# Kernel tuning notes

Hardware: AMD Instinct MI355X
Metric: run time of the kernel (lower is better)

The kernel has to match this reference:

```python
import jax, jax.numpy as jnp
import numpy as np

B, T, IN, H = 512, 1024, 1, 64


def setup_inputs() -> dict:
    key = jax.random.key(0)
    ks = jax.random.split(key, 7)
    s = 1.0 / np.sqrt(H)  # PyTorch LSTM init range
    u = lambda k, shape: jax.random.uniform(k, shape, jnp.float32, -s, s)
    return {
        "x": jax.random.normal(ks[0], (B, T, IN), jnp.float32),
        "W_ih": u(ks[1], (4 * H, IN)),
        "W_hh": u(ks[2], (4 * H, H)),
        "b_ih": u(ks[3], (4 * H,)),
        "b_hh": u(ks[4], (4 * H,)),
        "W_lin": u(ks[5], (1, H)),
        "b_lin": u(ks[6], (1,)),
    }


def reference(x, W_ih, W_hh, b_ih, b_hh, W_lin, b_lin):
    # x: [B, T, IN] (batch_first). Identity quantizers => plain LSTM math.
    Bsz = x.shape[0]
    Hs = W_hh.shape[1]
    bias = b_ih + b_hh  # fold the two bias vectors once
    xs = jnp.swapaxes(x, 0, 1)  # [T, B, IN] for scan over time
    h0 = jnp.zeros((Bsz, Hs), x.dtype)
    c0 = jnp.zeros((Bsz, Hs), x.dtype)

    def step(carry, xt):
        h, c = carry
        gates = xt @ W_ih.T + h @ W_hh.T + bias  # [B, 4H]
        i, f, g, o = jnp.split(gates, 4, axis=-1)  # PyTorch gate order i,f,g,o
        i = jax.nn.sigmoid(i)
        f = jax.nn.sigmoid(f)
        g = jnp.tanh(g)
        o = jax.nn.sigmoid(o)
        c_new = f * c + i * g
        h_new = o * jnp.tanh(c_new)
        return (h_new, c_new), None

    (h_final, _), _ = jax.lax.scan(step, (h0, c0), xs)
    # final_hidden_states.squeeze(0) -> [B, H]; linear -> [B, 1]; view(-1) -> [B]
    return (h_final @ W_lin.T + b_lin).reshape(-1)
```

## Files before the change

### kernel.cpp

```cpp
#include <hip/hip_runtime.h>


#define TLEN 1024
#define HID  64

__device__ __forceinline__ float fast_sigmoid(float x) {
    return __builtin_amdgcn_rcpf(1.0f + __expf(-x));
}
__device__ __forceinline__ float fast_tanh(float x) {
    return __builtin_fmaf(2.0f, fast_sigmoid(2.0f * x), -1.0f);
}

__global__ __launch_bounds__(256, 2)
void qlstm_kernel(const float* __restrict__ x,
                  const float* __restrict__ W_ih,
                  const float* __restrict__ W_hh,
                  const float* __restrict__ b_ih,
                  const float* __restrict__ b_hh,
                  const float* __restrict__ W_lin,
                  const float* __restrict__ b_lin,
                  float* __restrict__ out)
{
    const int b   = blockIdx.x;
    const int tid = threadIdx.x;
    const int w   = tid >> 6;
    const int l   = tid & 63;

    __shared__ __align__(16) float xs[TLEN];
    __shared__ __align__(16) float hs4[4][HID];
    __shared__ __align__(16) float act[2][4][HID];

    ((float4*)xs)[tid] = ((const float4*)(x + (size_t)b * TLEN))[tid];

    const int row = w * HID + l;
    const float4* Wr = (const float4*)(W_hh + (size_t)row * HID);
    float4 wq[16];
    #pragma unroll
    for (int q = 0; q < 16; ++q) wq[q] = Wr[q];

    const float u    = W_ih[row];
    const float bias = b_ih[row] + b_hh[row];
    const float wlin = W_lin[l];

    float c = 0.0f, h = 0.0f;
    hs4[w][l] = 0.0f;
    __syncthreads();

    for (int t = 0; t < TLEN; ++t) {
        const int p = t & 1;
        const float xt = xs[t];

        float acc = __builtin_fmaf(xt, u, bias);
        #pragma unroll
        for (int q = 0; q < 16; ++q) {
            const float4 hk = *(const float4*)&hs4[w][4 * q];
            acc = __builtin_fmaf(hk.x, wq[q].x, acc);
            acc = __builtin_fmaf(hk.y, wq[q].y, acc);
            acc = __builtin_fmaf(hk.z, wq[q].z, acc);
            acc = __builtin_fmaf(hk.w, wq[q].w, acc);
        }

        const float a = (w == 2) ? fast_tanh(acc) : fast_sigmoid(acc);
        act[p][w][l] = a;
        __syncthreads();

        const float ai = act[p][0][l];
        const float af = act[p][1][l];
        const float ag = act[p][2][l];
        const float ao = act[p][3][l];
        c = __builtin_fmaf(af, c, ai * ag);
        h = ao * fast_tanh(c);
        hs4[w][l] = h;
    }

    if (w == 0) {
        float v = h * wlin;
        #pragma unroll
        for (int off = 32; off > 0; off >>= 1)
            v += __shfl_down(v, off, 64);
        if (l == 0) out[b] = v + b_lin[0];
    }
}

extern "C" void kernel_launch(void* const* d_in, const int* in_sizes, int n_in,
                              void* d_out, int out_size, void* d_ws, size_t ws_size,
                              hipStream_t stream) {
    const float* x     = (const float*)d_in[0];
    const float* W_ih  = (const float*)d_in[1];
    const float* W_hh  = (const float*)d_in[2];
    const float* b_ih  = (const float*)d_in[3];
    const float* b_hh  = (const float*)d_in[4];
    const float* W_lin = (const float*)d_in[5];
    const float* b_lin = (const float*)d_in[6];
    float* out = (float*)d_out;

    const int B = out_size;
    qlstm_kernel<<<B, 256, 0, stream>>>(x, W_ih, W_hh, b_ih, b_hh, W_lin, b_lin, out);
}
```

Measured before the change: 584.3 us.

## Split each gate dot product across two half-waves with 512 threads per block

Doubles the block to 512 threads so each gate row's 64-long dot product over h is split between two half-wavefronts of 32 lanes, combined with a cross-lane xor shuffle. Each lane keeps half as many W_hh registers and uses four independent accumulators to shorten the serial FMA chain per step. Activations are stored as interleaved [HID][4] so the cell update reads all four gates with one float4 load. The cost is extra shuffle and wave overhead plus redundant cell-state computation across eight waves, and lower occupancy headroom from 512-thread blocks.

```diff
diff --git a/kernel.cpp b/kernel.cpp
--- a/kernel.cpp
+++ b/kernel.cpp
@@ -11,7 +11,7 @@
     return __builtin_fmaf(2.0f, fast_sigmoid(2.0f * x), -1.0f);
 }
 
-__global__ __launch_bounds__(256, 2)
+__global__ __launch_bounds__(512, 4)
 void qlstm_kernel(const float* __restrict__ x,
                   const float* __restrict__ W_ih,
                   const float* __restrict__ W_hh,
@@ -25,52 +25,73 @@
     const int tid = threadIdx.x;
     const int w   = tid >> 6;
     const int l   = tid & 63;
+    const int lr  = l & 31;
+    const int kh  = l >> 5;
+    const int g   = w >> 1;
+    const int row = w * 32 + lr;
+    const int k0  = kh * 32;
 
     __shared__ __align__(16) float xs[TLEN];
-    __shared__ __align__(16) float hs4[4][HID];
-    __shared__ __align__(16) float act[2][4][HID];
+    __shared__ __align__(16) float hs[8][HID];
+    __shared__ __align__(16) float act[2][HID][4];
 
-    ((float4*)xs)[tid] = ((const float4*)(x + (size_t)b * TLEN))[tid];
+    ((float2*)xs)[tid] = ((const float2*)(x + (size_t)b * TLEN))[tid];
 
-    const int row = w * HID + l;
-    const float4* Wr = (const float4*)(W_hh + (size_t)row * HID);
-    float4 wq[16];
+    const float4* Wr = (const float4*)(W_hh + (size_t)row * HID + k0);
+    float4 wq[8];
     #pragma unroll
-    for (int q = 0; q < 16; ++q) wq[q] = Wr[q];
+    for (int q = 0; q < 8; ++q) wq[q] = Wr[q];
 
     const float u    = W_ih[row];
     const float bias = b_ih[row] + b_hh[row];
     const float wlin = W_lin[l];
 
     float c = 0.0f, h = 0.0f;
-    hs4[w][l] = 0.0f;
+    hs[w][l] = 0.0f;
     __syncthreads();
 
     for (int t = 0; t < TLEN; ++t) {
         const int p = t & 1;
         const float xt = xs[t];
+        const float base = __builtin_fmaf(xt, u, bias);
 
-        float acc = __builtin_fmaf(xt, u, bias);
+        float acc0 = (kh == 0) ? base : 0.0f;
+        float acc1 = 0.0f, acc2 = 0.0f, acc3 = 0.0f;
         #pragma unroll
-        for (int q = 0; q < 16; ++q) {
-            const float4 hk = *(const float4*)&hs4[w][4 * q];
-            acc = __builtin_fmaf(hk.x, wq[q].x, acc);
-            acc = __builtin_fmaf(hk.y, wq[q].y, acc);
-            acc = __builtin_fmaf(hk.z, wq[q].z, acc);
-            acc = __builtin_fmaf(hk.w, wq[q].w, acc);
+        for (int q = 0; q < 8; q += 4) {
+            const float4 ha = *(const float4*)&hs[w][k0 + 4 * (q + 0)];
+            const float4 hb = *(const float4*)&hs[w][k0 + 4 * (q + 1)];
+            const float4 hc = *(const float4*)&hs[w][k0 + 4 * (q + 2)];
+            const float4 hd = *(const float4*)&hs[w][k0 + 4 * (q + 3)];
+            acc0 = __builtin_fmaf(ha.x, wq[q + 0].x, acc0);
+            acc0 = __builtin_fmaf(ha.y, wq[q + 0].y, acc0);
+            acc0 = __builtin_fmaf(ha.z, wq[q + 0].z, acc0);
+            acc0 = __builtin_fmaf(ha.w, wq[q + 0].w, acc0);
+            acc1 = __builtin_fmaf(hb.x, wq[q + 1].x, acc1);
+            acc1 = __builtin_fmaf(hb.y, wq[q + 1].y, acc1);
+            acc1 = __builtin_fmaf(hb.z, wq[q + 1].z, acc1);
+            acc1 = __builtin_fmaf(hb.w, wq[q + 1].w, acc1);
+            acc2 = __builtin_fmaf(hc.x, wq[q + 2].x, acc2);
+            acc2 = __builtin_fmaf(hc.y, wq[q + 2].y, acc2);
+            acc2 = __builtin_fmaf(hc.z, wq[q + 2].z, acc2);
+            acc2 = __builtin_fmaf(hc.w, wq[q + 2].w, acc2);
+            acc3 = __builtin_fmaf(hd.x, wq[q + 3].x, acc3);
+            acc3 = __builtin_fmaf(hd.y, wq[q + 3].y, acc3);
+            acc3 = __builtin_fmaf(hd.z, wq[q + 3].z, acc3);
+            acc3 = __builtin_fmaf(hd.w, wq[q + 3].w, acc3);
         }
+        float accv = (acc0 + acc1) + (acc2 + acc3);
+        accv += __shfl_xor(accv, 32, 64);
 
-        const float a = (w == 2) ? fast_tanh(acc) : fast_sigmoid(acc);
-        act[p][w][l] = a;
+        const float a = (g == 2) ? fast_tanh(accv) : fast_sigmoid(accv);
+        if (lr == l)
+            act[p][(w & 1) * 32 + lr][g] = a;
         __syncthreads();
 
-        const float ai = act[p][0][l];
-        const float af = act[p][1][l];
-        const float ag = act[p][2][l];
-        const float ao = act[p][3][l];
-        c = __builtin_fmaf(af, c, ai * ag);
-        h = ao * fast_tanh(c);
-        hs4[w][l] = h;
+        const float4 a4 = *(const float4*)&act[p][l][0];
+        c = __builtin_fmaf(a4.y, c, a4.x * a4.z);
+        h = a4.w * fast_tanh(c);
+        hs[w][l] = h;
     }
 
     if (w == 0) {
@@ -95,5 +116,5 @@
     float* out = (float*)d_out;
 
     const int B = out_size;
-    qlstm_kernel<<<B, 256, 0, stream>>>(x, W_ih, W_hh, b_ih, b_hh, W_lin, b_lin, out);
+    qlstm_kernel<<<B, 512, 0, stream>>>(x, W_ih, W_hh, b_ih, b_hh, W_lin, b_lin, out);
 }
```

Measured after the change: 605.7 us. 3.7% more time.

## Remap gate rows so each wave owns whole units and exchange gates via shuffles

Applied to the files above, without the earlier changes.

Each wave now holds all four gates for 16 hidden units, so the i/f/g/o values are gathered within the wave with cross-lane shuffles. This replaces the shared-memory act buffer and lets the loop drop one of its two barriers per step. The hidden state is double-buffered in a single shared array, and the dot product uses packed 2-wide FMAs with four independent accumulators to shorten the dependency chain. The gate activation is made branchless through per-lane scale and offset constants. The cost is that all four lane groups compute the cell update redundantly and extra shuffle instructions sit on the serial critical path.

```diff
diff --git a/kernel.cpp b/kernel.cpp
--- a/kernel.cpp
+++ b/kernel.cpp
@@ -1,14 +1,13 @@
 #include <hip/hip_runtime.h>
 
+
+typedef float v2f __attribute__((ext_vector_type(2)));
 
 #define TLEN 1024
 #define HID  64
 
 __device__ __forceinline__ float fast_sigmoid(float x) {
     return __builtin_amdgcn_rcpf(1.0f + __expf(-x));
-}
-__device__ __forceinline__ float fast_tanh(float x) {
-    return __builtin_fmaf(2.0f, fast_sigmoid(2.0f * x), -1.0f);
 }
 
 __global__ __launch_bounds__(256, 2)
@@ -21,60 +20,82 @@
                   const float* __restrict__ b_lin,
                   float* __restrict__ out)
 {
-    const int b   = blockIdx.x;
-    const int tid = threadIdx.x;
-    const int w   = tid >> 6;
-    const int l   = tid & 63;
+    const int b    = blockIdx.x;
+    const int tid  = threadIdx.x;
+    const int w    = tid >> 6;
+    const int l    = tid & 63;
+    const int u16  = l & 15;
+    const int gt   = l >> 4;
+    const int unit = w * 16 + u16;
+    const int row  = gt * HID + unit;
 
     __shared__ __align__(16) float xs[TLEN];
-    __shared__ __align__(16) float hs4[4][HID];
-    __shared__ __align__(16) float act[2][4][HID];
+    __shared__ __align__(16) float hs[2][HID];
 
     ((float4*)xs)[tid] = ((const float4*)(x + (size_t)b * TLEN))[tid];
 
-    const int row = w * HID + l;
-    const float4* Wr = (const float4*)(W_hh + (size_t)row * HID);
-    float4 wq[16];
+    v2f w2[32];
+    const v2f* Wr = (const v2f*)(W_hh + (size_t)row * HID);
     #pragma unroll
-    for (int q = 0; q < 16; ++q) wq[q] = Wr[q];
+    for (int q = 0; q < 32; ++q) w2[q] = Wr[q];
 
-    const float u    = W_ih[row];
+    const float uw   = W_ih[row];
     const float bias = b_ih[row] + b_hh[row];
-    const float wlin = W_lin[l];
 
-    float c = 0.0f, h = 0.0f;
-    hs4[w][l] = 0.0f;
+    const bool  isg = (gt == 2);
+    const float s_  = isg ? 2.0f : 1.0f;
+    const float m_  = isg ? 2.0f : 1.0f;
+    const float d_  = isg ? -1.0f : 0.0f;
+    const bool  lead = (gt == 0);
+    const bool  fi   = (gt < 2);
+
+    float c = 0.0f;
+    if (tid < HID) hs[0][tid] = 0.0f;
     __syncthreads();
 
     for (int t = 0; t < TLEN; ++t) {
         const int p = t & 1;
         const float xt = xs[t];
+        const float base = __builtin_fmaf(xt, uw, bias);
 
-        float acc = __builtin_fmaf(xt, u, bias);
+        v2f a0 = {base, 0.0f}, a1 = {0.0f, 0.0f}, a2 = {0.0f, 0.0f}, a3 = {0.0f, 0.0f};
+        const float4* hp = (const float4*)&hs[p][0];
         #pragma unroll
-        for (int q = 0; q < 16; ++q) {
-            const float4 hk = *(const float4*)&hs4[w][4 * q];
-            acc = __builtin_fmaf(hk.x, wq[q].x, acc);
-            acc = __builtin_fmaf(hk.y, wq[q].y, acc);
-            acc = __builtin_fmaf(hk.z, wq[q].z, acc);
-            acc = __builtin_fmaf(hk.w, wq[q].w, acc);
+        for (int q = 0; q < 16; q += 2) {
+            const float4 h0 = hp[q];
+            const float4 h1 = hp[q + 1];
+            const v2f hA = {h0.x, h0.y}, hB = {h0.z, h0.w};
+            const v2f hC = {h1.x, h1.y}, hD = {h1.z, h1.w};
+            a0 = __builtin_elementwise_fma(hA, w2[2 * q + 0], a0);
+            a1 = __builtin_elementwise_fma(hB, w2[2 * q + 1], a1);
+            a2 = __builtin_elementwise_fma(hC, w2[2 * q + 2], a2);
+            a3 = __builtin_elementwise_fma(hD, w2[2 * q + 3], a3);
         }
+        const v2f s2 = (a0 + a1) + (a2 + a3);
+        const float acc = s2.x + s2.y;
 
-        const float a = (w == 2) ? fast_tanh(acc) : fast_sigmoid(acc);
-        act[p][w][l] = a;
+        const float a = __builtin_fmaf(m_, fast_sigmoid(s_ * acc), d_);
+
+        const float b16  = __shfl_xor(a, 16, 64);
+        const float lo   = (gt & 1) ? b16 : a;
+        const float hi   = (gt & 1) ? a   : b16;
+        const float lo32 = __shfl_xor(lo, 32, 64);
+        const float hi32 = __shfl_xor(hi, 32, 64);
+        const float ig = fi ? lo   : lo32;
+        const float fg = fi ? hi   : hi32;
+        const float gg = fi ? lo32 : lo;
+        const float og = fi ? hi32 : hi;
+
+        c = __builtin_fmaf(fg, c, ig * gg);
+        const float th = __builtin_fmaf(2.0f, fast_sigmoid(2.0f * c), -1.0f);
+        const float h  = og * th;
+        if (lead) hs[p ^ 1][unit] = h;
+
         __syncthreads();
-
-        const float ai = act[p][0][l];
-        const float af = act[p][1][l];
-        const float ag = act[p][2][l];
-        const float ao = act[p][3][l];
-        c = __builtin_fmaf(af, c, ai * ag);
-        h = ao * fast_tanh(c);
-        hs4[w][l] = h;
     }
 
     if (w == 0) {
-        float v = h * wlin;
+        float v = hs[0][l] * W_lin[l];
         #pragma unroll
         for (int off = 32; off > 0; off >>= 1)
             v += __shfl_down(v, off, 64);
```

After: 606.2 us. +3.7%, slower.

## Use two-wave blocks with readlane h broadcast and packed FMA gate matvec

Applied to the files above, without the earlier changes.

Shrinks each block from four wavefronts (one per gate) to two, with each lane computing two gate rows held in registers as packed pairs. The hidden state is broadcast with readlane into scalar registers instead of going through LDS, and the matvec uses v_pk_fma_f32 with scalar operands, split across four accumulators. Only activations are exchanged between the two waves via LDS, which cuts shared-memory traffic and halves the waves taking part in each barrier. The cost is 64 readlanes per step, double the per-lane register footprint, and lower occupancy.

```diff
diff --git a/kernel.cpp b/kernel.cpp
--- a/kernel.cpp
+++ b/kernel.cpp
@@ -1,5 +1,7 @@
 #include <hip/hip_runtime.h>
 
+
+typedef float v2f __attribute__((ext_vector_type(2)));
 
 #define TLEN 1024
 #define HID  64
@@ -11,7 +13,7 @@
     return __builtin_fmaf(2.0f, fast_sigmoid(2.0f * x), -1.0f);
 }
 
-__global__ __launch_bounds__(256, 2)
+__global__ __launch_bounds__(128, 1)
 void qlstm_kernel(const float* __restrict__ x,
                   const float* __restrict__ W_ih,
                   const float* __restrict__ W_hh,
@@ -26,51 +28,84 @@
     const int w   = tid >> 6;
     const int l   = tid & 63;
 
-    __shared__ __align__(16) float xs[TLEN];
-    __shared__ __align__(16) float hs4[4][HID];
-    __shared__ __align__(16) float act[2][4][HID];
+    __shared__ __align__(16) float  xs[TLEN];
+    __shared__ __align__(8)  float2 axc[2][2][HID];
 
-    ((float4*)xs)[tid] = ((const float4*)(x + (size_t)b * TLEN))[tid];
+    {
+        const float4* xsrc = (const float4*)(x + (size_t)b * TLEN);
+        ((float4*)xs)[tid]       = xsrc[tid];
+        ((float4*)xs)[128 + tid] = xsrc[128 + tid];
+    }
 
-    const int row = w * HID + l;
-    const float4* Wr = (const float4*)(W_hh + (size_t)row * HID);
-    float4 wq[16];
-    #pragma unroll
-    for (int q = 0; q < 16; ++q) wq[q] = Wr[q];
+    const int r0 = (2 * w) * HID + l;
+    const int r1 = (2 * w + 1) * HID + l;
+    v2f wg2[64];
+    {
+        const float4* p0 = (const float4*)(W_hh + (size_t)r0 * HID);
+        const float4* p1 = (const float4*)(W_hh + (size_t)r1 * HID);
+        #pragma unroll
+        for (int k4 = 0; k4 < 16; ++k4) {
+            const float4 a = p0[k4];
+            const float4 c4 = p1[k4];
+            wg2[4 * k4 + 0] = (v2f){a.x, c4.x};
+            wg2[4 * k4 + 1] = (v2f){a.y, c4.y};
+            wg2[4 * k4 + 2] = (v2f){a.z, c4.z};
+            wg2[4 * k4 + 3] = (v2f){a.w, c4.w};
+        }
+    }
 
-    const float u    = W_ih[row];
-    const float bias = b_ih[row] + b_hh[row];
+    const v2f u2    = (v2f){W_ih[r0], W_ih[r1]};
+    const v2f bias2 = (v2f){b_ih[r0] + b_hh[r0], b_ih[r1] + b_hh[r1]};
     const float wlin = W_lin[l];
 
+    const float sA = (w == 1) ? 2.0f : 1.0f;
+    const float mA = (w == 1) ? 2.0f : 1.0f;
+    const float dA = (w == 1) ? -1.0f : 0.0f;
+
     float c = 0.0f, h = 0.0f;
-    hs4[w][l] = 0.0f;
     __syncthreads();
 
     for (int t = 0; t < TLEN; ++t) {
         const int p = t & 1;
         const float xt = xs[t];
 
-        float acc = __builtin_fmaf(xt, u, bias);
+        const int hbits = __float_as_int(h);
+        v2f hp[32];
         #pragma unroll
-        for (int q = 0; q < 16; ++q) {
-            const float4 hk = *(const float4*)&hs4[w][4 * q];
-            acc = __builtin_fmaf(hk.x, wq[q].x, acc);
-            acc = __builtin_fmaf(hk.y, wq[q].y, acc);
-            acc = __builtin_fmaf(hk.z, wq[q].z, acc);
-            acc = __builtin_fmaf(hk.w, wq[q].w, acc);
+        for (int q = 0; q < 32; ++q) {
+            hp[q].x = __int_as_float(__builtin_amdgcn_readlane(hbits, 2 * q));
+            hp[q].y = __int_as_float(__builtin_amdgcn_readlane(hbits, 2 * q + 1));
         }
 
-        const float a = (w == 2) ? fast_tanh(acc) : fast_sigmoid(acc);
-        act[p][w][l] = a;
+        v2f a0 = {0.0f, 0.0f}, a1 = {0.0f, 0.0f};
+        v2f a2 = {0.0f, 0.0f}, a3 = {0.0f, 0.0f};
+        #pragma unroll
+        for (int q = 0; q < 32; q += 2) {
+            asm("v_pk_fma_f32 %0, %1, %2, %0 op_sel:[0,0,0] op_sel_hi:[0,1,1]"
+                : "+v"(a0) : "s"(hp[q]),     "v"(wg2[2 * q + 0]));
+            asm("v_pk_fma_f32 %0, %1, %2, %0 op_sel:[1,0,0] op_sel_hi:[1,1,1]"
+                : "+v"(a1) : "s"(hp[q]),     "v"(wg2[2 * q + 1]));
+            asm("v_pk_fma_f32 %0, %1, %2, %0 op_sel:[0,0,0] op_sel_hi:[0,1,1]"
+                : "+v"(a2) : "s"(hp[q + 1]), "v"(wg2[2 * q + 2]));
+            asm("v_pk_fma_f32 %0, %1, %2, %0 op_sel:[1,0,0] op_sel_hi:[1,1,1]"
+                : "+v"(a3) : "s"(hp[q + 1]), "v"(wg2[2 * q + 3]));
+        }
+        v2f gate = (a0 + a1) + (a2 + a3);
+        gate.x = __builtin_fmaf(xt, u2.x, gate.x + bias2.x);
+        gate.y = __builtin_fmaf(xt, u2.y, gate.y + bias2.y);
+
+        const float ax = __builtin_fmaf(mA, fast_sigmoid(sA * gate.x), dA);
+        const float ay = fast_sigmoid(gate.y);
+
+        axc[p][w][l] = make_float2(ax, ay);
         __syncthreads();
-
-        const float ai = act[p][0][l];
-        const float af = act[p][1][l];
-        const float ag = act[p][2][l];
-        const float ao = act[p][3][l];
-        c = __builtin_fmaf(af, c, ai * ag);
-        h = ao * fast_tanh(c);
-        hs4[w][l] = h;
+        const float2 oth = axc[p][w ^ 1][l];
+        const float ig = w ? oth.x : ax;
+        const float fg = w ? oth.y : ay;
+        const float gg = w ? ax   : oth.x;
+        const float og = w ? ay   : oth.y;
+        c = __builtin_fmaf(fg, c, ig * gg);
+        h = og * fast_tanh(c);
     }
 
     if (w == 0) {
@@ -95,5 +130,5 @@
     float* out = (float*)d_out;
 
     const int B = out_size;
-    qlstm_kernel<<<B, 256, 0, stream>>>(x, W_ih, W_hh, b_ih, b_hh, W_lin, b_lin, out);
+    qlstm_kernel<<<B, 128, 0, stream>>>(x, W_ih, W_hh, b_ih, b_hh, W_lin, b_lin, out);
 }
```

Result: slower. 771.0 us (+32.0%).
